# Kernel tuning notes

Hardware: AMD Instinct MI355X
Metric: run time of the kernel (lower is better)

## Reference

```python
import jax, jax.numpy as jnp
import numpy as np

KH, KW = 11, 11
H, W = 6144, 6144


def setup_inputs() -> dict:
    key = jax.random.key(0)
    k1, k2 = jax.random.split(key)
    X = jax.random.normal(k1, (H, W), dtype=jnp.float32)
    weight = jax.random.uniform(k2, (KH, KW), dtype=jnp.float32)
    bias = jnp.zeros((1,), dtype=jnp.float32)
    return {"X": X, "weight": weight, "bias": bias}


def reference(X, weight, bias):
    # valid 2D cross-correlation: out[i,j] = sum(X[i:i+kh, j:j+kw] * K) + bias
    lhs = X[None, None]            # (1, 1, H, W)
    rhs = weight[None, None]       # (1, 1, kh, kw)  cross-correlation (no flip)
    out = jax.lax.conv_general_dilated(
        lhs, rhs,
        window_strides=(1, 1),
        padding="VALID",
        dimension_numbers=("NCHW", "OIHW", "NCHW"),
    )[0, 0]                         # (H-kh+1, W-kw+1)
    return out + bias[0]
```

## Files before the change

### kernel.cpp

```cpp
#include <hip/hip_runtime.h>

typedef _Float16 half8 __attribute__((ext_vector_type(8)));
typedef __fp16  fp16x2 __attribute__((ext_vector_type(2)));
typedef float f32x4 __attribute__((ext_vector_type(4)));

#define HH 6144
#define WW 6144
#define KH 11
#define KW 11
#define OH (HH - KH + 1)
#define OW (WW - KW + 1)

#define BROWS 32
#define BCOLS 128
#define SR 42
#define SCH 36
#define ROWB 576
#define A_TASKS 1512
#define A_PAD 1536
#define B_SLOTS 448
#define B_BYTES 7168
#define TOT_WAVETASKS 31
#define B_OFF 24576
#define LDSB 31744
#define CV_TASKS 756

#define TILES_X 48
#define TILES_Y 192
#define NWG (TILES_X * TILES_Y)

__global__ void build_B_kernel(const float* __restrict__ Wt,
                               _Float16* __restrict__ Bc) {
    const int t = (int)blockIdx.x * 256 + (int)threadIdx.x;
    if (t < B_SLOTS * 8) {
        const int e    = t & 7;
        const int slot = t >> 3;
        const int kb   = slot / 40;
        const int s    = slot - kb * 40;
        float v = 0.f;
        if (kb < KH) {
            const int d = s + e - 15;
            if (d >= 0 && d < KW) v = Wt[kb * KW + d];
        }
        Bc[t] = (_Float16)v;
    }
}

union pk2 { fp16x2 h; unsigned int u; };
static __device__ __forceinline__ unsigned int cvt2(float a, float b) {
#if defined(__has_builtin) && __has_builtin(__builtin_amdgcn_cvt_pkrtz)
    pk2 r; r.h = __builtin_amdgcn_cvt_pkrtz(a, b);
#else
    pk2 r; r.h[0] = (__fp16)a; r.h[1] = (__fp16)b;
#endif
    return r.u;
}

__global__ __launch_bounds__(256, 5)
void conv2d_dma3_kernel(const float* __restrict__ X,
                        const _Float16* __restrict__ Bc,
                        const float* __restrict__ bias,
                        float* __restrict__ out)
{
    __shared__ __align__(16) char lds[LDSB];

    const int bid = (int)blockIdx.x;
    const int sb  = (bid & 7) * (NWG / 8) + (bid >> 3);
    const int txt = sb % TILES_X;
    const int tyt = sb / TILES_X;

    const int x0 = txt * BCOLS;
    const int y0 = tyt * BROWS;
    const int tid = (int)threadIdx.x;
    const int lane = tid & 63;
    const int wv = tid >> 6;
    const int n  = lane & 15;
    const int h  = lane >> 4;
    const int rt = wv & 1;
    const int cs = wv >> 1;
    const float bv = bias[0];

    const bool interior = (txt < TILES_X - 1) && (tyt < TILES_Y - 1);

    if (interior) {
        #pragma unroll
        for (int k = 0; k < 8; ++k) {
            const int wabs = k * 4 + wv;
            if (wabs < TOT_WAVETASKS) {
                char* ldst = lds + wabs * 1024;
                const void* src;
                if (wabs < 24) {
                    const int t = wabs * 64 + lane;
                    int r = t / SCH;
                    const int j = t - r * SCH;
                    if (r > SR - 1) r = SR - 1;
                    src = (const void*)(X + (size_t)(y0 + r) * WW + (x0 + 4 * j));
                } else {
                    const int tb = (wabs - 24) * 64 + lane;
                    src = (const void*)((const char*)Bc + (size_t)tb * 16);
                }
                __builtin_amdgcn_global_load_lds(
                    (const __attribute__((address_space(1))) void*)src,
                    (__attribute__((address_space(3))) void*)ldst,
                    16, 0, 0);
            }
        }
    } else {
        #pragma unroll 1
        for (int k = 0; k < 8; ++k) {
            const int wabs = k * 4 + wv;
            if (wabs < TOT_WAVETASKS) {
                const int t = wabs * 64 + lane;
                if (wabs < 24) {
                    int r = t / SCH;
                    const int j = t - r * SCH;
                    if (r > SR - 1) r = SR - 1;
                    const int gy = y0 + r;
                    const int gx = x0 + 4 * j;
                    f32x4 v = {0.f, 0.f, 0.f, 0.f};
                    if (gy < HH) {
                        const float* rp = X + (size_t)gy * WW;
                        if (gx + 3 < WW) {
                            v = *reinterpret_cast<const f32x4*>(rp + gx);
                        } else {
                            if (gx + 0 < WW) v[0] = rp[gx + 0];
                            if (gx + 1 < WW) v[1] = rp[gx + 1];
                            if (gx + 2 < WW) v[2] = rp[gx + 2];
                        }
                    }
                    *reinterpret_cast<f32x4*>(lds + (size_t)t * 16) = v;
                } else {
                    const int tb = t - A_PAD;
                    *reinterpret_cast<uint4*>(lds + (size_t)t * 16) =
                        *reinterpret_cast<const uint4*>((const char*)Bc + (size_t)tb * 16);
                }
            }
        }
    }

    __syncthreads();

    f32x4 CV[3][2];
    #pragma unroll
    for (int it = 0; it < 3; ++it) {
        const int idx = it * 256 + tid;
        if (idx < CV_TASKS) {
            const int r = idx / 18;
            const int m = idx - r * 18;
            const char* frow = lds + (size_t)(r * SCH + 2 * m) * 16;
            CV[it][0] = *reinterpret_cast<const f32x4*>(frow);
            CV[it][1] = *reinterpret_cast<const f32x4*>(frow + 16);
        }
    }

    __syncthreads();

    #pragma unroll
    for (int it = 0; it < 3; ++it) {
        const int idx = it * 256 + tid;
        if (idx < CV_TASKS) {
            const int r = idx / 18;
            const int m = idx - r * 18;
            union { unsigned int u[4]; uint4 q; } fr;
            fr.u[0] = cvt2(CV[it][0][0], CV[it][0][1]);
            fr.u[1] = cvt2(CV[it][0][2], CV[it][0][3]);
            fr.u[2] = cvt2(CV[it][1][0], CV[it][1][1]);
            fr.u[3] = cvt2(CV[it][1][2], CV[it][1][3]);
            *reinterpret_cast<uint4*>(
                lds + (size_t)r * ROWB + (r & 7) * 32 + m * 16) = fr.q;
        }
    }

    f32x4 acc[4];
    #pragma unroll
    for (int c = 0; c < 4; ++c) acc[c] = (f32x4){bv, bv, bv, bv};

    __syncthreads();

    const char* abase = lds + (16 * rt + n) * ROWB + 128 * cs + 16 * h;
    const char* bbase = lds + B_OFF + (8 * h - n + 15) * 16;
    #pragma unroll
    for (int kb = 0; kb < 11; ++kb) {
        const half8 bf = *reinterpret_cast<const half8*>(bbase + kb * 640);
        const char* arow = abase + kb * ROWB + ((n + kb) & 7) * 32;
        #pragma unroll
        for (int c = 0; c < 4; ++c) {
            half8 a = *reinterpret_cast<const half8*>(arow + 32 * c);
            acc[c] = __builtin_amdgcn_mfma_f32_16x16x32_f16(a, bf, acc[c], 0, 0, 0);
        }
    }

    const int orow0 = y0 + 16 * rt + 4 * h;
    const int ocol0 = x0 + 64 * cs + n;
    if (interior) {
        #pragma unroll
        for (int r = 0; r < 4; ++r) {
            float* op = out + (size_t)(orow0 + r) * OW + ocol0;
            #pragma unroll
            for (int c = 0; c < 4; ++c)
                op[16 * c] = acc[c][r];
        }
    } else {
        #pragma unroll
        for (int r = 0; r < 4; ++r) {
            if (orow0 + r < OH) {
                float* op = out + (size_t)(orow0 + r) * OW + ocol0;
                #pragma unroll
                for (int c = 0; c < 4; ++c)
                    if (ocol0 + 16 * c < OW) op[16 * c] = acc[c][r];
            }
        }
    }
}

extern "C" void kernel_launch(void* const* d_in, const int* in_sizes, int n_in,
                              void* d_out, int out_size, void* d_ws, size_t ws_size,
                              hipStream_t stream) {
    const float* X    = (const float*)d_in[0];
    const float* Wt   = (const float*)d_in[1];
    const float* bias = (const float*)d_in[2];
    float* out        = (float*)d_out;
    _Float16* Bc      = (_Float16*)d_ws;

    build_B_kernel<<<dim3(14), dim3(256), 0, stream>>>(Wt, Bc);
    conv2d_dma3_kernel<<<dim3(NWG), dim3(256), 0, stream>>>(X, Bc, bias, out);
}
```

Before: 72.20 us.

## Build weight fragments in-kernel and compact fp16 LDS layout to shrink shared memory

Removes the separate weight-preparation kernel. Each block now builds the fp16 banded weight matrix itself from the raw float weights and writes it into LDS. The fp16 input tile moves to a dense 304-byte row stride without the XOR-style swizzle, so LDS per block drops from about 31 KB to 24 KB and launch bounds go up to 6 blocks per CU. The cost is redundant per-block weight loads and conversion (3584 elements per block), plus possible LDS bank conflicts from the unswizzled layout.

Measured after the change: 72.89 us. No clear change (+1.0%).

```diff
diff --git a/kernel.cpp b/kernel.cpp
--- a/kernel.cpp
+++ b/kernel.cpp
@@ -15,36 +15,18 @@
 #define BCOLS 128
 #define SR 42
 #define SCH 36
-#define ROWB 576
+#define F_ROWB 576
+#define H_ROWB 304
 #define A_TASKS 1512
 #define A_PAD 1536
-#define B_SLOTS 448
+#define B_OFF 12768
 #define B_BYTES 7168
-#define TOT_WAVETASKS 31
-#define B_OFF 24576
-#define LDSB 31744
+#define LDSB 24576
 #define CV_TASKS 756
 
 #define TILES_X 48
 #define TILES_Y 192
 #define NWG (TILES_X * TILES_Y)
-
-__global__ void build_B_kernel(const float* __restrict__ Wt,
-                               _Float16* __restrict__ Bc) {
-    const int t = (int)blockIdx.x * 256 + (int)threadIdx.x;
-    if (t < B_SLOTS * 8) {
-        const int e    = t & 7;
-        const int slot = t >> 3;
-        const int kb   = slot / 40;
-        const int s    = slot - kb * 40;
-        float v = 0.f;
-        if (kb < KH) {
-            const int d = s + e - 15;
-            if (d >= 0 && d < KW) v = Wt[kb * KW + d];
-        }
-        Bc[t] = (_Float16)v;
-    }
-}
 
 union pk2 { fp16x2 h; unsigned int u; };
 static __device__ __forceinline__ unsigned int cvt2(float a, float b) {
@@ -56,9 +38,9 @@
     return r.u;
 }
 
-__global__ __launch_bounds__(256, 5)
-void conv2d_dma3_kernel(const float* __restrict__ X,
-                        const _Float16* __restrict__ Bc,
+__global__ __launch_bounds__(256, 6)
+void conv2d_dma4_kernel(const float* __restrict__ X,
+                        const float* __restrict__ Wt,
                         const float* __restrict__ bias,
                         float* __restrict__ out)
 {
@@ -84,57 +66,41 @@
 
     if (interior) {
         #pragma unroll
-        for (int k = 0; k < 8; ++k) {
+        for (int k = 0; k < 6; ++k) {
             const int wabs = k * 4 + wv;
-            if (wabs < TOT_WAVETASKS) {
-                char* ldst = lds + wabs * 1024;
-                const void* src;
-                if (wabs < 24) {
-                    const int t = wabs * 64 + lane;
-                    int r = t / SCH;
-                    const int j = t - r * SCH;
-                    if (r > SR - 1) r = SR - 1;
-                    src = (const void*)(X + (size_t)(y0 + r) * WW + (x0 + 4 * j));
-                } else {
-                    const int tb = (wabs - 24) * 64 + lane;
-                    src = (const void*)((const char*)Bc + (size_t)tb * 16);
-                }
-                __builtin_amdgcn_global_load_lds(
-                    (const __attribute__((address_space(1))) void*)src,
-                    (__attribute__((address_space(3))) void*)ldst,
-                    16, 0, 0);
-            }
+            char* ldst = lds + wabs * 1024;
+            const int t = wabs * 64 + lane;
+            int r = t / SCH;
+            const int j = t - r * SCH;
+            if (r > SR - 1) r = SR - 1;
+            const void* src = (const void*)(X + (size_t)(y0 + r) * WW + (x0 + 4 * j));
+            __builtin_amdgcn_global_load_lds(
+                (const __attribute__((address_space(1))) void*)src,
+                (__attribute__((address_space(3))) void*)ldst,
+                16, 0, 0);
         }
     } else {
         #pragma unroll 1
-        for (int k = 0; k < 8; ++k) {
+        for (int k = 0; k < 6; ++k) {
             const int wabs = k * 4 + wv;
-            if (wabs < TOT_WAVETASKS) {
-                const int t = wabs * 64 + lane;
-                if (wabs < 24) {
-                    int r = t / SCH;
-                    const int j = t - r * SCH;
-                    if (r > SR - 1) r = SR - 1;
-                    const int gy = y0 + r;
-                    const int gx = x0 + 4 * j;
-                    f32x4 v = {0.f, 0.f, 0.f, 0.f};
-                    if (gy < HH) {
-                        const float* rp = X + (size_t)gy * WW;
-                        if (gx + 3 < WW) {
-                            v = *reinterpret_cast<const f32x4*>(rp + gx);
-                        } else {
-                            if (gx + 0 < WW) v[0] = rp[gx + 0];
-                            if (gx + 1 < WW) v[1] = rp[gx + 1];
-                            if (gx + 2 < WW) v[2] = rp[gx + 2];
-                        }
-                    }
-                    *reinterpret_cast<f32x4*>(lds + (size_t)t * 16) = v;
+            const int t = wabs * 64 + lane;
+            int r = t / SCH;
+            const int j = t - r * SCH;
+            if (r > SR - 1) r = SR - 1;
+            const int gy = y0 + r;
+            const int gx = x0 + 4 * j;
+            f32x4 v = {0.f, 0.f, 0.f, 0.f};
+            if (gy < HH) {
+                const float* rp = X + (size_t)gy * WW;
+                if (gx + 3 < WW) {
+                    v = *reinterpret_cast<const f32x4*>(rp + gx);
                 } else {
-                    const int tb = t - A_PAD;
-                    *reinterpret_cast<uint4*>(lds + (size_t)t * 16) =
-                        *reinterpret_cast<const uint4*>((const char*)Bc + (size_t)tb * 16);
+                    if (gx + 0 < WW) v[0] = rp[gx + 0];
+                    if (gx + 1 < WW) v[1] = rp[gx + 1];
+                    if (gx + 2 < WW) v[2] = rp[gx + 2];
                 }
             }
+            *reinterpret_cast<f32x4*>(lds + (size_t)t * 16) = v;
         }
     }
 
@@ -167,7 +133,27 @@
             fr.u[2] = cvt2(CV[it][1][0], CV[it][1][1]);
             fr.u[3] = cvt2(CV[it][1][2], CV[it][1][3]);
             *reinterpret_cast<uint4*>(
-                lds + (size_t)r * ROWB + (r & 7) * 32 + m * 16) = fr.q;
+                lds + (size_t)r * H_ROWB + m * 16) = fr.q;
+        }
+    }
+
+    {
+        const int base = tid * 14;
+        float v[14];
+        #pragma unroll
+        for (int i = 0; i < 14; ++i) {
+            const int idx  = base + i;
+            const int slot = idx >> 3;
+            const int e    = idx & 7;
+            const int kb   = slot / 40;
+            const int s    = slot - kb * 40;
+            const int d    = s + e - 15;
+            v[i] = (kb < KH && d >= 0 && d < KW) ? Wt[kb * KW + d] : 0.f;
+        }
+        #pragma unroll
+        for (int i = 0; i < 7; ++i) {
+            *reinterpret_cast<unsigned int*>(lds + B_OFF + (size_t)(base + 2 * i) * 2)
+                = cvt2(v[2 * i], v[2 * i + 1]);
         }
     }
 
@@ -177,12 +163,12 @@
 
     __syncthreads();
 
-    const char* abase = lds + (16 * rt + n) * ROWB + 128 * cs + 16 * h;
+    const char* abase = lds + (16 * rt + n) * H_ROWB + 128 * cs + 16 * h;
     const char* bbase = lds + B_OFF + (8 * h - n + 15) * 16;
     #pragma unroll
     for (int kb = 0; kb < 11; ++kb) {
         const half8 bf = *reinterpret_cast<const half8*>(bbase + kb * 640);
-        const char* arow = abase + kb * ROWB + ((n + kb) & 7) * 32;
+        const char* arow = abase + kb * H_ROWB;
         #pragma unroll
         for (int c = 0; c < 4; ++c) {
             half8 a = *reinterpret_cast<const half8*>(arow + 32 * c);
@@ -220,8 +206,6 @@
     const float* Wt   = (const float*)d_in[1];
     const float* bias = (const float*)d_in[2];
     float* out        = (float*)d_out;
-    _Float16* Bc      = (_Float16*)d_ws;
-
-    build_B_kernel<<<dim3(14), dim3(256), 0, stream>>>(Wt, Bc);
-    conv2d_dma3_kernel<<<dim3(NWG), dim3(256), 0, stream>>>(X, Bc, bias, out);
+
+    conv2d_dma4_kernel<<<dim3(NWG), dim3(256), 0, stream>>>(X, Wt, bias, out);
 }
```

## Shrink tile to 96 columns and reuse LDS for weights to raise occupancy

Applied to the files above, without the earlier changes.

Narrows each workgroup tile from 128 to 96 output columns and drops the row swizzle in the fp16 staging buffer. The weight matrix now loads after the fp32 input has been read into registers, placed in the freed LDS region, which cuts LDS per block from about 31 KB to 19 KB. Launch bounds go from 5 to 8 blocks per SM. The aim is more resident waves to hide memory latency, at the cost of more halo overfetch per output, more workgroups, and possible LDS bank conflicts from the unswizzled layout.

After: 71.55 us. Within noise of the previous version (-0.9%).

```diff
diff --git a/kernel.cpp b/kernel.cpp
--- a/kernel.cpp
+++ b/kernel.cpp
@@ -12,27 +12,26 @@
 #define OW (WW - KW + 1)
 
 #define BROWS 32
-#define BCOLS 128
+#define BCOLS 96
 #define SR 42
-#define SCH 36
-#define ROWB 576
-#define A_TASKS 1512
-#define A_PAD 1536
-#define B_SLOTS 448
+#define SCH 28
+#define F_ROWB 448
+#define H_ROWB 224
+#define A_TASKS 1176
+#define A_WAVES 19
+#define B_LDS 9408
 #define B_BYTES 7168
-#define TOT_WAVETASKS 31
-#define B_OFF 24576
-#define LDSB 31744
-#define CV_TASKS 756
-
-#define TILES_X 48
+#define LDSB 19456
+#define CV_TASKS 588
+
+#define TILES_X 64
 #define TILES_Y 192
 #define NWG (TILES_X * TILES_Y)
 
 __global__ void build_B_kernel(const float* __restrict__ Wt,
                                _Float16* __restrict__ Bc) {
     const int t = (int)blockIdx.x * 256 + (int)threadIdx.x;
-    if (t < B_SLOTS * 8) {
+    if (t < 448 * 8) {
         const int e    = t & 7;
         const int slot = t >> 3;
         const int kb   = slot / 40;
@@ -56,8 +55,8 @@
     return r.u;
 }
 
-__global__ __launch_bounds__(256, 5)
-void conv2d_dma3_kernel(const float* __restrict__ X,
+__global__ __launch_bounds__(256, 8)
+void conv2d_dma5_kernel(const float* __restrict__ X,
                         const _Float16* __restrict__ Bc,
                         const float* __restrict__ bias,
                         float* __restrict__ out)
@@ -84,21 +83,15 @@
 
     if (interior) {
         #pragma unroll
-        for (int k = 0; k < 8; ++k) {
+        for (int k = 0; k < 5; ++k) {
             const int wabs = k * 4 + wv;
-            if (wabs < TOT_WAVETASKS) {
+            if (wabs < A_WAVES) {
                 char* ldst = lds + wabs * 1024;
-                const void* src;
-                if (wabs < 24) {
-                    const int t = wabs * 64 + lane;
-                    int r = t / SCH;
-                    const int j = t - r * SCH;
-                    if (r > SR - 1) r = SR - 1;
-                    src = (const void*)(X + (size_t)(y0 + r) * WW + (x0 + 4 * j));
-                } else {
-                    const int tb = (wabs - 24) * 64 + lane;
-                    src = (const void*)((const char*)Bc + (size_t)tb * 16);
-                }
+                const int t = wabs * 64 + lane;
+                int r = t / SCH;
+                const int j = t - r * SCH;
+                if (r > SR - 1) r = SR - 1;
+                const void* src = (const void*)(X + (size_t)(y0 + r) * WW + (x0 + 4 * j));
                 __builtin_amdgcn_global_load_lds(
                     (const __attribute__((address_space(1))) void*)src,
                     (__attribute__((address_space(3))) void*)ldst,
@@ -107,33 +100,27 @@
         }
     } else {
         #pragma unroll 1
-        for (int k = 0; k < 8; ++k) {
+        for (int k = 0; k < 5; ++k) {
             const int wabs = k * 4 + wv;
-            if (wabs < TOT_WAVETASKS) {
+            if (wabs < A_WAVES) {
                 const int t = wabs * 64 + lane;
-                if (wabs < 24) {
-                    int r = t / SCH;
-                    const int j = t - r * SCH;
-                    if (r > SR - 1) r = SR - 1;
-                    const int gy = y0 + r;
-                    const int gx = x0 + 4 * j;
-                    f32x4 v = {0.f, 0.f, 0.f, 0.f};
-                    if (gy < HH) {
-                        const float* rp = X + (size_t)gy * WW;
-                        if (gx + 3 < WW) {
-                            v = *reinterpret_cast<const f32x4*>(rp + gx);
-                        } else {
-                            if (gx + 0 < WW) v[0] = rp[gx + 0];
-                            if (gx + 1 < WW) v[1] = rp[gx + 1];
-                            if (gx + 2 < WW) v[2] = rp[gx + 2];
-                        }
+                int r = t / SCH;
+                const int j = t - r * SCH;
+                if (r > SR - 1) r = SR - 1;
+                const int gy = y0 + r;
+                const int gx = x0 + 4 * j;
+                f32x4 v = {0.f, 0.f, 0.f, 0.f};
+                if (gy < HH) {
+                    const float* rp = X + (size_t)gy * WW;
+                    if (gx + 3 < WW) {
+                        v = *reinterpret_cast<const f32x4*>(rp + gx);
+                    } else {
+                        if (gx + 0 < WW) v[0] = rp[gx + 0];
+                        if (gx + 1 < WW) v[1] = rp[gx + 1];
+                        if (gx + 2 < WW) v[2] = rp[gx + 2];
                     }
-                    *reinterpret_cast<f32x4*>(lds + (size_t)t * 16) = v;
-                } else {
-                    const int tb = t - A_PAD;
-                    *reinterpret_cast<uint4*>(lds + (size_t)t * 16) =
-                        *reinterpret_cast<const uint4*>((const char*)Bc + (size_t)tb * 16);
                 }
+                *reinterpret_cast<f32x4*>(lds + (size_t)t * 16) = v;
             }
         }
     }
@@ -145,59 +132,83 @@
     for (int it = 0; it < 3; ++it) {
         const int idx = it * 256 + tid;
         if (idx < CV_TASKS) {
-            const int r = idx / 18;
-            const int m = idx - r * 18;
-            const char* frow = lds + (size_t)(r * SCH + 2 * m) * 16;
+            const int r = idx / 14;
+            const int m = idx - r * 14;
+            const char* frow = lds + (size_t)r * F_ROWB + m * 32;
             CV[it][0] = *reinterpret_cast<const f32x4*>(frow);
             CV[it][1] = *reinterpret_cast<const f32x4*>(frow + 16);
         }
     }
 
     __syncthreads();
+
+    if (interior) {
+        #pragma unroll
+        for (int k = 0; k < 2; ++k) {
+            const int wb = k * 4 + wv;
+            if (wb < 7) {
+                char* ldst = lds + B_LDS + wb * 1024;
+                const void* src = (const void*)((const char*)Bc + (size_t)(wb * 64 + lane) * 16);
+                __builtin_amdgcn_global_load_lds(
+                    (const __attribute__((address_space(1))) void*)src,
+                    (__attribute__((address_space(3))) void*)ldst,
+                    16, 0, 0);
+            }
+        }
+    } else {
+        #pragma unroll
+        for (int k = 0; k < 2; ++k) {
+            const int wb = k * 4 + wv;
+            if (wb < 7) {
+                const int t = wb * 64 + lane;
+                *reinterpret_cast<uint4*>(lds + B_LDS + (size_t)t * 16) =
+                    *reinterpret_cast<const uint4*>((const char*)Bc + (size_t)t * 16);
+            }
+        }
+    }
 
     #pragma unroll
     for (int it = 0; it < 3; ++it) {
         const int idx = it * 256 + tid;
         if (idx < CV_TASKS) {
-            const int r = idx / 18;
-            const int m = idx - r * 18;
+            const int r = idx / 14;
+            const int m = idx - r * 14;
             union { unsigned int u[4]; uint4 q; } fr;
             fr.u[0] = cvt2(CV[it][0][0], CV[it][0][1]);
             fr.u[1] = cvt2(CV[it][0][2], CV[it][0][3]);
             fr.u[2] = cvt2(CV[it][1][0], CV[it][1][1]);
             fr.u[3] = cvt2(CV[it][1][2], CV[it][1][3]);
-            *reinterpret_cast<uint4*>(
-                lds + (size_t)r * ROWB + (r & 7) * 32 + m * 16) = fr.q;
-        }
-    }
-
-    f32x4 acc[4];
-    #pragma unroll
-    for (int c = 0; c < 4; ++c) acc[c] = (f32x4){bv, bv, bv, bv};
+            *reinterpret_cast<uint4*>(lds + (size_t)r * H_ROWB + m * 16) = fr.q;
+        }
+    }
+
+    f32x4 acc[3];
+    #pragma unroll
+    for (int c = 0; c < 3; ++c) acc[c] = (f32x4){bv, bv, bv, bv};
 
     __syncthreads();
 
-    const char* abase = lds + (16 * rt + n) * ROWB + 128 * cs + 16 * h;
-    const char* bbase = lds + B_OFF + (8 * h - n + 15) * 16;
+    const char* abase = lds + (16 * rt + n) * H_ROWB + 96 * cs + 16 * h;
+    const char* bbase = lds + B_LDS + (8 * h - n + 15) * 16;
     #pragma unroll
     for (int kb = 0; kb < 11; ++kb) {
         const half8 bf = *reinterpret_cast<const half8*>(bbase + kb * 640);
-        const char* arow = abase + kb * ROWB + ((n + kb) & 7) * 32;
-        #pragma unroll
-        for (int c = 0; c < 4; ++c) {
+        const char* arow = abase + kb * H_ROWB;
+        #pragma unroll
+        for (int c = 0; c < 3; ++c) {
             half8 a = *reinterpret_cast<const half8*>(arow + 32 * c);
             acc[c] = __builtin_amdgcn_mfma_f32_16x16x32_f16(a, bf, acc[c], 0, 0, 0);
         }
     }
 
     const int orow0 = y0 + 16 * rt + 4 * h;
-    const int ocol0 = x0 + 64 * cs + n;
+    const int ocol0 = x0 + 48 * cs + n;
     if (interior) {
         #pragma unroll
         for (int r = 0; r < 4; ++r) {
             float* op = out + (size_t)(orow0 + r) * OW + ocol0;
             #pragma unroll
-            for (int c = 0; c < 4; ++c)
+            for (int c = 0; c < 3; ++c)
                 op[16 * c] = acc[c][r];
         }
     } else {
@@ -206,7 +217,7 @@
             if (orow0 + r < OH) {
                 float* op = out + (size_t)(orow0 + r) * OW + ocol0;
                 #pragma unroll
-                for (int c = 0; c < 4; ++c)
+                for (int c = 0; c < 3; ++c)
                     if (ocol0 + 16 * c < OW) op[16 * c] = acc[c][r];
             }
         }
@@ -223,5 +234,5 @@
     _Float16* Bc      = (_Float16*)d_ws;
 
     build_B_kernel<<<dim3(14), dim3(256), 0, stream>>>(Wt, Bc);
-    conv2d_dma3_kernel<<<dim3(NWG), dim3(256), 0, stream>>>(X, Bc, bias, out);
-}
+    conv2d_dma5_kernel<<<dim3(NWG), dim3(256), 0, stream>>>(X, Bc, bias, out);
+}
```
